# Kernel tuning notes

Measured on AMD Instinct MI355X. Metric: run time of the kernel, lower is better.

## Reference

```python
import jax, jax.numpy as jnp
import numpy as np

N, E = 50000, 800000
H, V, ED = 128, 32, 64
EH = 2 * H + 2 * V          # edge MLP hidden = 320
EO = 2 * H + 2 * V          # edge MLP out (H+H+V+V) = 320
NH = 2 * H + V              # node MLP hidden = 288
NO = H + V                  # node MLP out = 160


def _ln(x, g, b, eps=1e-5):
    m = x.mean(-1, keepdims=True)
    v = ((x - m) ** 2).mean(-1, keepdims=True)
    return (x - m) * jax.lax.rsqrt(v + eps) * g + b


def setup_inputs() -> dict:
    key = jax.random.key(0)
    ks = jax.random.split(key, 12)
    s = 0.05
    return {
        "scalar_state": jax.random.normal(ks[0], (N, H), jnp.float32),
        "vector_state": jax.random.normal(ks[1], (N, 3, V), jnp.float32),
        "edge_attr": jax.random.normal(ks[2], (E, ED), jnp.float32),
        "edge_vector": jax.random.normal(ks[3], (E, 3), jnp.float32),
        "sn_g": jnp.ones((H,), jnp.float32), "sn_b": jnp.zeros((H,), jnp.float32),
        "pn_g": jnp.ones((H,), jnp.float32), "pn_b": jnp.zeros((H,), jnp.float32),
        "e_w1": jax.random.normal(ks[4], (2 * H + ED, EH), jnp.float32) * s,
        "e_b1": jnp.zeros((EH,), jnp.float32),
        "e_w2": jax.random.normal(ks[5], (EH, EO), jnp.float32) * s,
        "e_b2": jnp.zeros((EO,), jnp.float32),
        "n_w1": jax.random.normal(ks[6], (H + V, NH), jnp.float32) * s,
        "n_b1": jnp.zeros((NH,), jnp.float32),
        "n_w2": jax.random.normal(ks[7], (NH, NO), jnp.float32) * s,
        "n_b2": jnp.zeros((NO,), jnp.float32),
        "edge_index": jax.random.randint(ks[8], (2, E), 0, N, jnp.int64),
    }


def reference(scalar_state, vector_state, edge_attr, edge_vector,
              sn_g, sn_b, pn_g, pn_b,
              e_w1, e_b1, e_w2, e_b2,
              n_w1, n_b1, n_w2, n_b2, edge_index):
    tgt = edge_index[0]
    src = edge_index[1]

    # LayerNorm is per-row, so normalize once then gather (same math as gather-then-norm)
    s_norm = _ln(scalar_state, sn_g, sn_b)
    edge_in = jnp.concatenate([s_norm[tgt], s_norm[src], edge_attr], axis=-1)  # [E, 2H+ED]
    h = jax.nn.silu(edge_in @ e_w1 + e_b1)
    upd = h @ e_w2 + e_b2                                                      # [E, 2H+2V]
    sm = upd[:, :H]
    sg = upd[:, H:2 * H]
    vg = upd[:, 2 * H:2 * H + V]
    ds = upd[:, 2 * H + V:]

    sm = sm * jax.nn.sigmoid(sg)                                               # scalar message [E,H]

    # F.normalize(edge_vector, dim=-1, eps=1e-8)
    ev_norm = jnp.sqrt((edge_vector ** 2).sum(-1, keepdims=True))
    unit = edge_vector / jnp.maximum(ev_norm, 1e-8)                            # [E,3]

    src_vec = vector_state[src] * jax.nn.sigmoid(vg)[:, None, :]               # [E,3,V]
    dir_vec = unit[:, :, None] * ds[:, None, :]                                # [E,3,V]
    vmsg = src_vec + dir_vec

    # mean aggregation (index_add / counts)
    counts = jax.ops.segment_sum(jnp.ones((E,), sm.dtype), tgt, num_segments=N)
    counts = jnp.maximum(counts, 1.0)
    s_upd = jax.ops.segment_sum(sm, tgt, num_segments=N) / counts[:, None]
    v_upd = jax.ops.segment_sum(vmsg.reshape(E, 3 * V), tgt, num_segments=N).reshape(N, 3, V) / counts[:, None, None]

    scalar_state = scalar_state + s_upd
    vector_state = vector_state + v_upd

    vnorm = jnp.sqrt(jnp.maximum((vector_state ** 2).sum(axis=1), 1e-8))       # [N,V]
    node_in = jnp.concatenate([_ln(scalar_state, pn_g, pn_b), vnorm], axis=-1)
    h2 = jax.nn.silu(node_in @ n_w1 + n_b1)
    nu = h2 @ n_w2 + n_b2                                                      # [N,H+V]
    scalar_delta = nu[:, :H]
    vector_scale = nu[:, H:]

    scalar_state = scalar_state + scalar_delta
    vector_state = vector_state * (1.0 + 0.1 * jnp.tanh(vector_scale))[:, None, :]
    return scalar_state, vector_state
```

## Files before the change

kernel.cpp:

```cpp
#include <hip/hip_runtime.h>

#define N_NODES 50000
#define N_EDGES 800000

typedef __attribute__((ext_vector_type(8))) short short8;
typedef __attribute__((ext_vector_type(4))) float floatx4;
typedef __attribute__((ext_vector_type(4))) unsigned int u32x4;
typedef unsigned short ushort_t;
typedef unsigned int uint_t;

__device__ __forceinline__ ushort_t f2bf(float f){
  unsigned u = __builtin_bit_cast(unsigned, f);
  u += 0x7fffu + ((u >> 16) & 1u);
  return (ushort_t)(u >> 16);
}
__device__ __forceinline__ float bf2f(ushort_t h){
  unsigned u = ((unsigned)h) << 16;
  return __builtin_bit_cast(float, u);
}
__device__ __forceinline__ uint_t pkbf(float lo, float hi){
#if __has_builtin(__builtin_amdgcn_cvt_pk_bf16_f32)
  typedef __attribute__((ext_vector_type(2))) __bf16 bf16x2;
  bf16x2 r = __builtin_amdgcn_cvt_pk_bf16_f32(lo, hi);
  return __builtin_bit_cast(uint_t, r);
#else
  return (uint_t)f2bf(lo) | ((uint_t)f2bf(hi) << 16);
#endif
}
__device__ __forceinline__ float sigm(float x){ return 1.f/(1.f+__expf(-x)); }
__device__ __forceinline__ float waveRed(float v){
  #pragma unroll
  for (int o=32;o>0;o>>=1) v += __shfl_xor(v,o);
  return v;
}
__device__ __forceinline__ int ldIdx(const int* __restrict__ idx, long long pos, int mode){
  return mode ? idx[pos*2] : idx[pos];
}
__device__ __forceinline__ short8 as_s8(u32x4 v){ return __builtin_bit_cast(short8, v); }

__device__ __forceinline__ void gl_lds16(const ushort_t* g, ushort_t* l){
  __builtin_amdgcn_global_load_lds(
    (const __attribute__((address_space(1))) unsigned int*)(unsigned long long)(uintptr_t)g,
    (__attribute__((address_space(3))) unsigned int*)(unsigned int)(uintptr_t)l,
    16, 0, 0);
}

__device__ __forceinline__ u32x4 bfadd8(u32x4 a, u32x4 b){
  u32x4 r;
  #pragma unroll
  for (int i=0;i<4;++i){
    float alo = __builtin_bit_cast(float, a[i]<<16);
    float ahi = __builtin_bit_cast(float, a[i]&0xffff0000u);
    float blo = __builtin_bit_cast(float, b[i]<<16);
    float bhi = __builtin_bit_cast(float, b[i]&0xffff0000u);
    r[i] = pkbf(alo+blo, ahi+bhi);
  }
  return r;
}
__device__ __forceinline__ short8 pack8(floatx4 x, floatx4 y){
  u32x4 u;
  u[0] = pkbf(x[0], x[1]); u[1] = pkbf(x[2], x[3]);
  u[2] = pkbf(y[0], y[1]); u[3] = pkbf(y[2], y[3]);
  return __builtin_bit_cast(short8, u);
}


__global__ void kDetect(const int* __restrict__ idx, int* __restrict__ flag){
  if (threadIdx.x==0 && blockIdx.x==0){
    int any = 0;
    for (int i=1;i<64;i+=2) any |= idx[i];
    *flag = (any==0) ? 1 : 0;
  }
}

__global__ void kLN(const float* __restrict__ s, const float* __restrict__ g,
                    const float* __restrict__ b, ushort_t* __restrict__ out, int N){
  int wid = threadIdx.x >> 6, lane = threadIdx.x & 63;
  int n = blockIdx.x*4 + wid;
  if (n >= N) return;
  float x0 = s[(size_t)n*128 + lane], x1 = s[(size_t)n*128 + 64 + lane];
  float sum = waveRed(x0 + x1);
  float sq  = waveRed(x0*x0 + x1*x1);
  float mean = sum * (1.f/128.f);
  float var  = sq * (1.f/128.f) - mean*mean;
  float rstd = rsqrtf(var + 1e-5f);
  out[(size_t)n*128 + lane]      = f2bf((x0-mean)*rstd*g[lane] + b[lane]);
  out[(size_t)n*128 + 64 + lane] = f2bf((x1-mean)*rstd*g[64+lane] + b[64+lane]);
}

__global__ void kReorder(const float* __restrict__ W, ushort_t* __restrict__ Wp,
                         int K, int OUT){
  int total = K*OUT;
  for (int o = blockIdx.x*blockDim.x + threadIdx.x; o < total; o += gridDim.x*blockDim.x){
    int j = o & 7; int rest = o >> 3;
    int nn = rest % OUT; int qk = rest / OUT;
    int q = qk & 3, kt = qk >> 2;
    int k = kt*32 + q*8 + j;
    Wp[o] = f2bf(W[(size_t)k*OUT + nn]);
  }
}

__global__ void kReorderAB(const float* __restrict__ W, ushort_t* __restrict__ Wp){
  int total = 128*640;
  for (int o = blockIdx.x*blockDim.x + threadIdx.x; o < total; o += gridDim.x*blockDim.x){
    int j = o & 7; int rest = o >> 3;
    int nn = rest % 640; int qk = rest / 640;
    int q = qk & 3, kt = qk >> 2;
    int k = kt*32 + q*8 + j;
    float v = (nn < 320) ? W[(size_t)k*320 + nn] : W[(size_t)(128+k)*320 + (nn-320)];
    Wp[o] = f2bf(v);
  }
}


__global__ void kHist(const int* __restrict__ idx, const int* __restrict__ flagp,
                      int* __restrict__ counts){
  int mode = *flagp;
  long long e = (long long)blockIdx.x*256 + threadIdx.x;
  if (e < N_EDGES) atomicAdd(&counts[ldIdx(idx, e, mode)], 1);
}

__global__ void kScanLocal(const int* __restrict__ counts, int* __restrict__ offsets,
                           int* __restrict__ bsum, int n){
  int tid = threadIdx.x, lane = tid & 63, wid = tid >> 6;
  int i = blockIdx.x*1024 + tid;
  int x = (i<n) ? counts[i] : 0;
  int v = x;
  #pragma unroll
  for (int o=1;o<64;o<<=1){ int t = __shfl_up(v,o); if (lane>=o) v += t; }
  __shared__ int ws[16];
  if (lane==63) ws[wid] = v;
  __syncthreads();
  if (wid==0){
    int s = (lane<16) ? ws[lane] : 0;
    #pragma unroll
    for (int o=1;o<16;o<<=1){ int t = __shfl_up(s,o); if (lane>=o) s += t; }
    if (lane<16) ws[lane] = s;
  }
  __syncthreads();
  int base = wid ? ws[wid-1] : 0;
  if (i<n) offsets[i] = base + v - x;
  if (tid==1023) bsum[blockIdx.x] = ws[15];
}
__global__ void kScanSums(const int* __restrict__ bsum, int* __restrict__ bbase, int nb){
  int lane = threadIdx.x;
  int x = (lane<nb) ? bsum[lane] : 0;
  int v = x;
  #pragma unroll
  for (int o=1;o<64;o<<=1){ int t = __shfl_up(v,o); if (lane>=o) v += t; }
  if (lane<nb) bbase[lane] = v - x;
}
__global__ void kScanAdd(int* __restrict__ offsets, int* __restrict__ cursor,
                         const int* __restrict__ bbase, int n){
  int i = blockIdx.x*1024 + threadIdx.x;
  if (i<n){ int v = offsets[i] + bbase[blockIdx.x]; offsets[i]=v; cursor[i]=v; }
}

__global__ void kScatter(const int* __restrict__ idx, const int* __restrict__ flagp,
                         int* __restrict__ cursor, const float* __restrict__ edge_vector,
                         int* __restrict__ sortedE, ushort_t* __restrict__ sortedT,
                         floatx4* __restrict__ aux){
  int mode = *flagp;
  long long e = (long long)blockIdx.x*256 + threadIdx.x;
  if (e < N_EDGES){
    int t = ldIdx(idx, e, mode);
    int s = ldIdx(idx, (long long)N_EDGES + e, mode);
    float ex = edge_vector[e*3], ey = edge_vector[e*3+1], ez = edge_vector[e*3+2];
    float inr = 1.f / fmaxf(sqrtf(ex*ex+ey*ey+ez*ez), 1e-8f);
    int pos = atomicAdd(&cursor[t], 1);
    sortedE[pos] = (int)e;
    sortedT[pos] = (ushort_t)t;
    floatx4 a; a[0] = __int_as_float(s); a[1] = ex*inr; a[2] = ey*inr; a[3] = ez*inr;
    aux[pos] = a;
  }
}

__global__ __launch_bounds__(256,2) void kNodeP(
  const ushort_t* __restrict__ s_norm, const ushort_t* __restrict__ Wabp,
  const float* __restrict__ b1, ushort_t* __restrict__ P)
{
  __shared__ u32x4 sA[1024];
  __shared__ u32x4 sB[2560];
  const int tid = threadIdx.x;
  const int lane = tid & 63, wid = tid >> 6;
  const int col = lane & 15, quad = lane >> 4;
  const int nb0 = blockIdx.x * 64;

  for (int i=0;i<4;++i){
    int d = i*256 + tid;
    int m=d&15, q=(d>>4)&3, mt=(d>>6)&3, kt=d>>8;
    int node = nb0 + mt*16 + m;
    u32x4 v = {0,0,0,0};
    if (node < N_NODES) v = *(const u32x4*)(s_norm + (size_t)node*128 + (kt*4+q)*8);
    sA[d] = v;
  }

  const floatx4 zz = {0.f,0.f,0.f,0.f};
  floatx4 acc[10][4];
  #pragma unroll
  for (int i=0;i<10;++i)
    #pragma unroll
    for (int j=0;j<4;++j) acc[i][j] = zz;

  for (int kt=0; kt<4; ++kt){
    for (int i=0;i<10;++i){
      int cb = i*256 + wid*64;
      gl_lds16(Wabp + ((size_t)kt*2560 + cb + lane)*8, (ushort_t*)&sB[cb]);
    }
    __syncthreads();
    short8 a[4];
    #pragma unroll
    for (int mt=0; mt<4; ++mt)
      a[mt] = as_s8(sA[((kt*4+mt)*4+quad)*16 + col]);
    #pragma unroll
    for (int nt=0; nt<10; ++nt){
      int n = wid*160 + nt*16 + col;
      short8 b = as_s8(sB[quad*640 + n]);
      #pragma unroll
      for (int mt=0; mt<4; ++mt)
        acc[nt][mt] = __builtin_amdgcn_mfma_f32_16x16x32_bf16(a[mt], b, acc[nt][mt], 0,0,0);
    }
    __syncthreads();
  }

  #pragma unroll
  for (int nt=0; nt<10; ++nt){
    int n = wid*160 + nt*16 + col;
    float bias = (n < 320) ? b1[n] : 0.f;
    #pragma unroll
    for (int mt=0; mt<4; ++mt)
      #pragma unroll
      for (int reg=0; reg<4; ++reg){
        int node = nb0 + mt*16 + quad*4 + reg;
        if (node < N_NODES)
          P[(size_t)node*640 + n] = f2bf(acc[nt][mt][reg] + bias);
      }
  }
}

__global__ __launch_bounds__(256,3) void kEdgeMLP(
    const ushort_t* __restrict__ P, const float* __restrict__ edge_attr,
    const ushort_t* __restrict__ W1cp, const ushort_t* __restrict__ W2p,
    const float* __restrict__ b2, const int* __restrict__ sortedE,
    const ushort_t* __restrict__ sortedT, const floatx4* __restrict__ aux,
    ushort_t* __restrict__ msg)
{
  __shared__ u32x4 sA[2560];
  __shared__ int sTgt[64], sSrc[64], sE[64];
  const int tid = threadIdx.x;
  const int lane = tid & 63, wid = tid >> 6;
  const int col = lane & 15, quad = lane >> 4;
  const long long p0 = (long long)blockIdx.x * 64;
  const int nb = wid * 80;

  if (tid < 64){
    sTgt[tid] = (int)sortedT[p0 + tid];
    sE[tid]   = sortedE[p0 + tid];
    sSrc[tid] = __float_as_int(aux[p0 + tid][0]);
  }
  __syncthreads();

  short8 aQ[2][4];
  #pragma unroll
  for (int kq=0; kq<2; ++kq)
    #pragma unroll
    for (int mt=0; mt<4; ++mt){
      const float* fp = edge_attr + (size_t)sE[mt*16+col]*64 + kq*32 + quad*8;
      aQ[kq][mt] = pack8(*(const floatx4*)fp, *(const floatx4*)(fp+4));
    }

  for (int i=0;i<10;++i){
    int d = i*256 + tid;
    int m=d&15, q=(d>>4)&3, mt=(d>>6)&3, kt=d>>8;
    int r = mt*16 + m;
    int n0 = kt*32 + q*8;
    u32x4 a = *(const u32x4*)(P + (size_t)sTgt[r]*640 + n0);
    u32x4 b = *(const u32x4*)(P + (size_t)sSrc[r]*640 + 320 + n0);
    sA[d] = bfadd8(a, b);
  }
  __syncthreads();

  const floatx4 zz = {0.f,0.f,0.f,0.f};
  floatx4 acc[5][4];
  #pragma unroll
  for (int i=0;i<5;++i)
    #pragma unroll
    for (int j=0;j<4;++j) acc[i][j] = zz;

  #pragma unroll
  for (int kq=0; kq<2; ++kq)
    #pragma unroll
    for (int nt=0; nt<5; ++nt){
      short8 b = as_s8(*(const u32x4*)(W1cp + ((size_t)(kq*4+quad)*320 + nb + nt*16 + col)*8));
      #pragma unroll
      for (int mt=0; mt<4; ++mt)
        acc[nt][mt] = __builtin_amdgcn_mfma_f32_16x16x32_bf16(aQ[kq][mt], b, acc[nt][mt], 0,0,0);
    }

  ushort_t* sH16 = (ushort_t*)sA;
  #pragma unroll
  for (int nt=0; nt<5; ++nt){
    int n = nb + nt*16 + col;
    int kt_h = n>>5, q_h = (n>>3)&3, j_h = n&7;
    #pragma unroll
    for (int mt=0; mt<4; ++mt)
      #pragma unroll
      for (int reg=0; reg<4; ++reg){
        int ml = quad*4 + reg;
        int a2 = (((kt_h*4 + mt)*4 + q_h)*16 + ml)*8 + j_h;
        float x = acc[nt][mt][reg] + bf2f(sH16[a2]);
        sH16[a2] = f2bf(x * sigm(x));
      }
  }
  #pragma unroll
  for (int i=0;i<5;++i)
    #pragma unroll
    for (int j=0;j<4;++j) acc[i][j] = zz;
  __syncthreads();

  const ushort_t* wb = W2p + ((size_t)quad*320 + nb + col)*8;
  for (int kt=0; kt<10; ++kt){
    short8 bfr[5];
    #pragma unroll
    for (int nt=0; nt<5; ++nt)
      bfr[nt] = as_s8(*(const u32x4*)(wb + (size_t)kt*10240 + nt*128));
    short8 a[4];
    #pragma unroll
    for (int mt=0; mt<4; ++mt)
      a[mt] = as_s8(sA[((kt*4+mt)*4+quad)*16 + col]);
    #pragma unroll
    for (int nt=0; nt<5; ++nt)
      #pragma unroll
      for (int mt=0; mt<4; ++mt)
        acc[nt][mt] = __builtin_amdgcn_mfma_f32_16x16x32_bf16(a[mt], bfr[nt], acc[nt][mt], 0,0,0);
  }
  __syncthreads();

  #pragma unroll
  for (int nt=0; nt<5; ++nt){
    int n = nb + nt*16 + col;
    float bias = b2[n];
    #pragma unroll
    for (int mt=0; mt<4; ++mt)
      #pragma unroll
      for (int reg=0; reg<4; ++reg){
        int mrow = mt*16 + quad*4 + reg;
        sH16[mrow*320 + n] = f2bf(acc[nt][mt][reg] + bias);
      }
  }
  __syncthreads();

  for (int pck = tid; pck < 6144; pck += 256){
    int r = pck / 96, u = pck % 96;
    float v0, v1;
    if (u < 64){
      int c0 = u*2;
      float a0 = bf2f(sH16[r*320 + c0]),   g0 = bf2f(sH16[r*320 + 128 + c0]);
      float a1 = bf2f(sH16[r*320 + c0+1]), g1 = bf2f(sH16[r*320 + 128 + c0+1]);
      v0 = a0 * sigm(g0); v1 = a1 * sigm(g1);
    } else if (u < 80){
      int vv = (u-64)*2;
      v0 = sigm(bf2f(sH16[r*320 + 256 + vv]));
      v1 = sigm(bf2f(sH16[r*320 + 256 + vv+1]));
    } else {
      int vv = (u-80)*2;
      v0 = bf2f(sH16[r*320 + 288 + vv]);
      v1 = bf2f(sH16[r*320 + 288 + vv+1]);
    }
    ((uint_t*)msg)[(size_t)(p0 + r)*96 + u] = pkbf(v0, v1);
  }
}

__global__ __launch_bounds__(128) void kAgg(
  const ushort_t* __restrict__ msg, const floatx4* __restrict__ aux,
  const int* __restrict__ counts, const int* __restrict__ offsets,
  const float* __restrict__ scalar_state, const float* __restrict__ vector_state,
  const float* __restrict__ pn_g, const float* __restrict__ pn_b,
  float* __restrict__ outS, float* __restrict__ outV, ushort_t* __restrict__ node_in)
{
  int n = blockIdx.x, t = threadIdx.x;
  int cnt = counts[n], start = offsets[n];
  int c = t >> 5, vv = t & 31;
  float accS = 0.f, accV = 0.f;
  for (int i=0; i<cnt; ++i){
    const ushort_t* row = msg + (size_t)(start+i)*192;
    accS += bf2f(row[t]);
    if (t < 96){
      floatx4 a = aux[start+i];
      int src = __float_as_int(a[0]);
      float sg  = bf2f(row[128+vv]);
      float dsv = bf2f(row[160+vv]);
      float sv = vector_state[(size_t)src*96 + t];
      float uc = (c==0) ? a[1] : (c==1) ? a[2] : a[3];
      accV += sv*sg + uc*dsv;
    }
  }
  float inv = 1.f / fmaxf((float)cnt, 1.f);
  __shared__ float lv[96];
  __shared__ float pS[2], pQ[2];
  float s1 = scalar_state[(size_t)n*128 + t] + accS*inv;
  outS[(size_t)n*128 + t] = s1;
  if (t < 96){
    float v1 = vector_state[(size_t)n*96 + t] + accV*inv;
    outV[(size_t)n*96 + t] = v1;
    lv[t] = v1;
  }
  float wsum = waveRed(s1), wsq = waveRed(s1*s1);
  if ((t&63)==0){ pS[t>>6]=wsum; pQ[t>>6]=wsq; }
  __syncthreads();
  float mean = (pS[0]+pS[1]) * (1.f/128.f);
  float var  = (pQ[0]+pQ[1]) * (1.f/128.f) - mean*mean;
  float rstd = rsqrtf(var + 1e-5f);
  node_in[(size_t)n*160 + t] = f2bf((s1-mean)*rstd*pn_g[t] + pn_b[t]);
  if (t < 32){
    float a = lv[t], b = lv[32+t], d = lv[64+t];
    float vn = sqrtf(fmaxf(a*a+b*b+d*d, 1e-8f));
    node_in[(size_t)n*160 + 128 + t] = f2bf(vn);
  }
}

__global__ __launch_bounds__(256,2) void kNodeMLP(
  const ushort_t* __restrict__ node_in, const ushort_t* __restrict__ W1np,
  const ushort_t* __restrict__ W2np, const float* __restrict__ b1,
  const float* __restrict__ b2, float* __restrict__ outS, float* __restrict__ outV)
{
  __shared__ u32x4 sA[640];
  __shared__ u32x4 sH[1152];
  const int tid = threadIdx.x;
  const int lane = tid & 63, wid = tid >> 6;
  const int col = lane & 15, quad = lane >> 4;
  const int wm = wid & 1, wn = wid >> 1;
  const int rbase = blockIdx.x * 32;

  for (int d = tid; d < 640; d += 256){
    int m = d & 15, q = (d>>4)&3, mtile = (d>>6)&1, kt = d>>7;
    int r = rbase + mtile*16 + m, cc = kt*4 + q;
    u32x4 v = {0,0,0,0};
    if (r < N_NODES) v = *(const u32x4*)(node_in + (size_t)r*160 + cc*8);
    sA[d] = v;
  }
  __syncthreads();

  const floatx4 zz = {0.f,0.f,0.f,0.f};
  floatx4 acc[9];
  #pragma unroll
  for (int i=0;i<9;++i) acc[i] = zz;

  for (int kt=0; kt<5; ++kt){
    short8 a = as_s8(sA[((kt*2+wm)*4+quad)*16 + col]);
    #pragma unroll
    for (int jt=0; jt<9; ++jt){
      int n = wn*144 + jt*16 + col;
      short8 b = as_s8(*(const u32x4*)(W1np + (size_t)kt*9216 + ((size_t)quad*288 + n)*8));
      acc[jt] = __builtin_amdgcn_mfma_f32_16x16x32_bf16(a, b, acc[jt], 0,0,0);
    }
  }
  ushort_t* sH16 = (ushort_t*)sH;
  #pragma unroll
  for (int jt=0; jt<9; ++jt){
    int n = wn*144 + jt*16 + col;
    float bias = b1[n];
    int kt_h = n>>5, q_h = (n>>3)&3, j_h = n&7;
    #pragma unroll
    for (int reg=0; reg<4; ++reg){
      int ml = quad*4 + reg;
      float x = acc[jt][reg] + bias;
      float s = x * sigm(x);
      int chunk = ((kt_h*2 + wm)*4 + q_h)*16 + ml;
      sH16[chunk*8 + j_h] = f2bf(s);
    }
  }
  __syncthreads();

  floatx4 acc2[5];
  #pragma unroll
  for (int i=0;i<5;++i) acc2[i] = zz;

  for (int kt=0; kt<9; ++kt){
    short8 a = as_s8(sH[((kt*2+wm)*4+quad)*16 + col]);
    #pragma unroll
    for (int jt=0; jt<5; ++jt){
      int n = wn*80 + jt*16 + col;
      short8 b = as_s8(*(const u32x4*)(W2np + (size_t)kt*5120 + ((size_t)quad*160 + n)*8));
      acc2[jt] = __builtin_amdgcn_mfma_f32_16x16x32_bf16(a, b, acc2[jt], 0,0,0);
    }
  }

  #pragma unroll
  for (int jt=0; jt<5; ++jt){
    int n = wn*80 + jt*16 + col;
    float bias = b2[n];
    #pragma unroll
    for (int reg=0; reg<4; ++reg){
      int ml = quad*4 + reg;
      int r = rbase + wm*16 + ml;
      if (r < N_NODES){
        float val = acc2[jt][reg] + bias;
        if (n < 128){
          float* o = outS + (size_t)r*128 + n;
          *o = *o + val;
        } else {
          int vv = n - 128;
          float f = 1.f + 0.1f * tanhf(val);
          float* o = outV + (size_t)r*96 + vv;
          o[0] *= f; o[32] *= f; o[64] *= f;
        }
      }
    }
  }
}


extern "C" void kernel_launch(void* const* d_in, const int* in_sizes, int n_in,
                              void* d_out, int out_size, void* d_ws, size_t ws_size,
                              hipStream_t stream)
{
  const float* scalar_state = (const float*)d_in[0];
  const float* vector_state = (const float*)d_in[1];
  const float* edge_attr    = (const float*)d_in[2];
  const float* edge_vector  = (const float*)d_in[3];
  const float* sn_g = (const float*)d_in[4];
  const float* sn_b = (const float*)d_in[5];
  const float* pn_g = (const float*)d_in[6];
  const float* pn_b = (const float*)d_in[7];
  const float* e_w1 = (const float*)d_in[8];
  const float* e_b1 = (const float*)d_in[9];
  const float* e_w2 = (const float*)d_in[10];
  const float* e_b2 = (const float*)d_in[11];
  const float* n_w1 = (const float*)d_in[12];
  const float* n_b1 = (const float*)d_in[13];
  const float* n_w2 = (const float*)d_in[14];
  const float* n_b2 = (const float*)d_in[15];
  const int*   eidx = (const int*)d_in[16];

  char* p = (char*)d_ws;
  auto take = [&](size_t bytes)->char*{
    char* r = p; p += (bytes + 255) & ~(size_t)255; return r;
  };
  int*      flag    = (int*)take(4);
  ushort_t* s_norm  = (ushort_t*)take((size_t)N_NODES*128*2);
  ushort_t* Wabp    = (ushort_t*)take((size_t)128*640*2);
  ushort_t* W1cp    = (ushort_t*)take((size_t)64*320*2);
  ushort_t* W2p     = (ushort_t*)take((size_t)320*320*2);
  ushort_t* W1np    = (ushort_t*)take((size_t)160*288*2);
  ushort_t* W2np    = (ushort_t*)take((size_t)288*160*2);
  int*      counts  = (int*)take((size_t)N_NODES*4);
  int*      offsets = (int*)take((size_t)N_NODES*4);
  int*      cursor  = (int*)take((size_t)N_NODES*4);
  int*      bsum    = (int*)take(64*4);
  int*      bbase   = (int*)take(64*4);
  int*      sortedE = (int*)take((size_t)N_EDGES*4);
  ushort_t* sortedT = (ushort_t*)take((size_t)N_EDGES*2);
  floatx4*  aux     = (floatx4*)take((size_t)N_EDGES*16);
  ushort_t* Pbuf    = (ushort_t*)take((size_t)N_NODES*640*2);
  ushort_t* msg     = (ushort_t*)take((size_t)N_EDGES*192*2);
  ushort_t* node_in = Pbuf;
  (void)ws_size; (void)in_sizes; (void)n_in; (void)out_size;

  float* outS = (float*)d_out;
  float* outV = outS + (size_t)N_NODES*128;

  kDetect<<<1, 64, 0, stream>>>(eidx, flag);
  kLN<<<(N_NODES+3)/4, 256, 0, stream>>>(scalar_state, sn_g, sn_b, s_norm, N_NODES);
  kReorderAB<<<160, 256, 0, stream>>>(e_w1, Wabp);
  kReorder<<<160, 256, 0, stream>>>(e_w1 + (size_t)256*320, W1cp, 64, 320);
  kReorder<<<160, 256, 0, stream>>>(e_w2, W2p, 320, 320);
  kReorder<<<160, 256, 0, stream>>>(n_w1, W1np, 160, 288);
  kReorder<<<160, 256, 0, stream>>>(n_w2, W2np, 288, 160);
  hipMemsetAsync(counts, 0, (size_t)N_NODES*4, stream);
  kHist<<<N_EDGES/256, 256, 0, stream>>>(eidx, flag, counts);
  int nsb = (N_NODES + 1023)/1024;
  kScanLocal<<<nsb, 1024, 0, stream>>>(counts, offsets, bsum, N_NODES);
  kScanSums<<<1, 64, 0, stream>>>(bsum, bbase, nsb);
  kScanAdd<<<nsb, 1024, 0, stream>>>(offsets, cursor, bbase, N_NODES);
  kScatter<<<N_EDGES/256, 256, 0, stream>>>(eidx, flag, cursor, edge_vector,
                                            sortedE, sortedT, aux);
  kNodeP<<<(N_NODES+63)/64, 256, 0, stream>>>(s_norm, Wabp, e_b1, Pbuf);
  kEdgeMLP<<<N_EDGES/64, 256, 0, stream>>>(Pbuf, edge_attr, W1cp, W2p,
                                           e_b2, sortedE, sortedT, aux, msg);
  kAgg<<<N_NODES, 128, 0, stream>>>(msg, aux, counts, offsets,
                                    scalar_state, vector_state,
                                    pn_g, pn_b, outS, outV, node_in);
  kNodeMLP<<<(N_NODES+31)/32, 256, 0, stream>>>(node_in, W1np, W2np, n_b1, n_b2, outS, outV);
}
```

Before: 1.237 ms.

## Remap edge MLP output columns so gating epilogue runs in registers

The edge MLP now gives each wave output columns so that the message column and its gate column (n and n+128) sit in the same lane's accumulators. The sigmoid gating and the bf16 message store can then be done straight from registers. This removes the LDS staging of the full 64x320 output, two block barriers and the repacking loop. It also loads edge indices straight into registers instead of through shared memory, and swaps in hardware rcp based sigmoid/tanh and native bf16 conversions. The trade-offs are narrow scattered 2-byte global stores of msg and slightly lower accuracy in the fast reciprocal and tanh.

```diff
diff --git a/kernel.cpp b/kernel.cpp
--- a/kernel.cpp
+++ b/kernel.cpp
@@ -6,28 +6,29 @@
 typedef __attribute__((ext_vector_type(8))) short short8;
 typedef __attribute__((ext_vector_type(4))) float floatx4;
 typedef __attribute__((ext_vector_type(4))) unsigned int u32x4;
+typedef __attribute__((ext_vector_type(2))) __bf16 bf16x2;
 typedef unsigned short ushort_t;
 typedef unsigned int uint_t;
 
+__device__ __forceinline__ uint_t pkbf(float lo, float hi){
+  bf16x2 v = { (__bf16)lo, (__bf16)hi };
+  return __builtin_bit_cast(uint_t, v);
+}
 __device__ __forceinline__ ushort_t f2bf(float f){
-  unsigned u = __builtin_bit_cast(unsigned, f);
-  u += 0x7fffu + ((u >> 16) & 1u);
-  return (ushort_t)(u >> 16);
+  return __builtin_bit_cast(ushort_t, (__bf16)f);
 }
 __device__ __forceinline__ float bf2f(ushort_t h){
   unsigned u = ((unsigned)h) << 16;
   return __builtin_bit_cast(float, u);
 }
-__device__ __forceinline__ uint_t pkbf(float lo, float hi){
-#if __has_builtin(__builtin_amdgcn_cvt_pk_bf16_f32)
-  typedef __attribute__((ext_vector_type(2))) __bf16 bf16x2;
-  bf16x2 r = __builtin_amdgcn_cvt_pk_bf16_f32(lo, hi);
-  return __builtin_bit_cast(uint_t, r);
-#else
-  return (uint_t)f2bf(lo) | ((uint_t)f2bf(hi) << 16);
-#endif
-}
-__device__ __forceinline__ float sigm(float x){ return 1.f/(1.f+__expf(-x)); }
+__device__ __forceinline__ float sigm(float x){
+  return __builtin_amdgcn_rcpf(1.f + __expf(-x));
+}
+__device__ __forceinline__ float tanh_f(float x){
+  float ax = fabsf(x);
+  float t = 1.f - 2.f*__builtin_amdgcn_rcpf(__expf(2.f*ax) + 1.f);
+  return copysignf(t, x);
+}
 __device__ __forceinline__ float waveRed(float v){
   #pragma unroll
   for (int o=32;o>0;o>>=1) v += __shfl_xor(v,o);
@@ -246,37 +247,40 @@
     ushort_t* __restrict__ msg)
 {
   __shared__ u32x4 sA[2560];
-  __shared__ int sTgt[64], sSrc[64], sE[64];
   const int tid = threadIdx.x;
   const int lane = tid & 63, wid = tid >> 6;
   const int col = lane & 15, quad = lane >> 4;
   const long long p0 = (long long)blockIdx.x * 64;
-  const int nb = wid * 80;
-
-  if (tid < 64){
-    sTgt[tid] = (int)sortedT[p0 + tid];
-    sE[tid]   = sortedE[p0 + tid];
-    sSrc[tid] = __float_as_int(aux[p0 + tid][0]);
-  }
-  __syncthreads();
+
+  int ncol[5];
+  ncol[0] = wid*32 + col;
+  ncol[1] = ncol[0] + 16;
+  ncol[2] = ncol[0] + 128;
+  ncol[3] = ncol[0] + 144;
+  ncol[4] = 256 + wid*16 + col;
+
+  int eId[4];
+  #pragma unroll
+  for (int mt=0;mt<4;++mt) eId[mt] = sortedE[p0 + mt*16 + col];
 
   short8 aQ[2][4];
   #pragma unroll
   for (int kq=0; kq<2; ++kq)
     #pragma unroll
     for (int mt=0; mt<4; ++mt){
-      const float* fp = edge_attr + (size_t)sE[mt*16+col]*64 + kq*32 + quad*8;
+      const float* fp = edge_attr + (size_t)eId[mt]*64 + kq*32 + quad*8;
       aQ[kq][mt] = pack8(*(const floatx4*)fp, *(const floatx4*)(fp+4));
     }
 
-  for (int i=0;i<10;++i){
-    int d = i*256 + tid;
-    int m=d&15, q=(d>>4)&3, mt=(d>>6)&3, kt=d>>8;
-    int r = mt*16 + m;
-    int n0 = kt*32 + q*8;
-    u32x4 a = *(const u32x4*)(P + (size_t)sTgt[r]*640 + n0);
-    u32x4 b = *(const u32x4*)(P + (size_t)sSrc[r]*640 + 320 + n0);
-    sA[d] = bfadd8(a, b);
+  {
+    const int r = wid*16 + col;
+    int tgt = (int)sortedT[p0 + r];
+    int src = __float_as_int(((const float*)aux)[(size_t)(p0 + r)*4]);
+    const u32x4* pT = (const u32x4*)(P + (size_t)tgt*640) + quad;
+    const u32x4* pS = (const u32x4*)(P + (size_t)src*640 + 320) + quad;
+    #pragma unroll
+    for (int i=0;i<10;++i)
+      sA[i*256 + tid] = bfadd8(pT[i*4], pS[i*4]);
   }
   __syncthreads();
 
@@ -291,7 +295,7 @@
   for (int kq=0; kq<2; ++kq)
     #pragma unroll
     for (int nt=0; nt<5; ++nt){
-      short8 b = as_s8(*(const u32x4*)(W1cp + ((size_t)(kq*4+quad)*320 + nb + nt*16 + col)*8));
+      short8 b = as_s8(*(const u32x4*)(W1cp + ((size_t)(kq*4+quad)*320 + ncol[nt])*8));
       #pragma unroll
       for (int mt=0; mt<4; ++mt)
         acc[nt][mt] = __builtin_amdgcn_mfma_f32_16x16x32_bf16(aQ[kq][mt], b, acc[nt][mt], 0,0,0);
@@ -300,16 +304,15 @@
   ushort_t* sH16 = (ushort_t*)sA;
   #pragma unroll
   for (int nt=0; nt<5; ++nt){
-    int n = nb + nt*16 + col;
-    int kt_h = n>>5, q_h = (n>>3)&3, j_h = n&7;
+    int n = ncol[nt];
+    ushort_t* hp = sH16 + (((n>>5)*256 + ((n>>3)&3)*16 + quad*4)*8 + (n&7));
     #pragma unroll
     for (int mt=0; mt<4; ++mt)
       #pragma unroll
       for (int reg=0; reg<4; ++reg){
-        int ml = quad*4 + reg;
-        int a2 = (((kt_h*4 + mt)*4 + q_h)*16 + ml)*8 + j_h;
-        float x = acc[nt][mt][reg] + bf2f(sH16[a2]);
-        sH16[a2] = f2bf(x * sigm(x));
+        int a2 = mt*512 + reg*8;
+        float x = acc[nt][mt][reg] + bf2f(hp[a2]);
+        hp[a2] = f2bf(x * sigm(x));
       }
   }
   #pragma unroll
@@ -318,12 +321,16 @@
     for (int j=0;j<4;++j) acc[i][j] = zz;
   __syncthreads();
 
-  const ushort_t* wb = W2p + ((size_t)quad*320 + nb + col)*8;
+  float b2c[5];
+  #pragma unroll
+  for (int nt=0;nt<5;++nt) b2c[nt] = b2[ncol[nt]];
+
+  const ushort_t* w2q = W2p + (size_t)quad*320*8;
   for (int kt=0; kt<10; ++kt){
     short8 bfr[5];
     #pragma unroll
     for (int nt=0; nt<5; ++nt)
-      bfr[nt] = as_s8(*(const u32x4*)(wb + (size_t)kt*10240 + nt*128));
+      bfr[nt] = as_s8(*(const u32x4*)(w2q + (size_t)kt*10240 + (size_t)ncol[nt]*8));
     short8 a[4];
     #pragma unroll
     for (int mt=0; mt<4; ++mt)
@@ -334,41 +341,23 @@
       for (int mt=0; mt<4; ++mt)
         acc[nt][mt] = __builtin_amdgcn_mfma_f32_16x16x32_bf16(a[mt], bfr[nt], acc[nt][mt], 0,0,0);
   }
-  __syncthreads();
-
-  #pragma unroll
-  for (int nt=0; nt<5; ++nt){
-    int n = nb + nt*16 + col;
-    float bias = b2[n];
-    #pragma unroll
-    for (int mt=0; mt<4; ++mt)
-      #pragma unroll
-      for (int reg=0; reg<4; ++reg){
-        int mrow = mt*16 + quad*4 + reg;
-        sH16[mrow*320 + n] = f2bf(acc[nt][mt][reg] + bias);
-      }
-  }
-  __syncthreads();
-
-  for (int pck = tid; pck < 6144; pck += 256){
-    int r = pck / 96, u = pck % 96;
-    float v0, v1;
-    if (u < 64){
-      int c0 = u*2;
-      float a0 = bf2f(sH16[r*320 + c0]),   g0 = bf2f(sH16[r*320 + 128 + c0]);
-      float a1 = bf2f(sH16[r*320 + c0+1]), g1 = bf2f(sH16[r*320 + 128 + c0+1]);
-      v0 = a0 * sigm(g0); v1 = a1 * sigm(g1);
-    } else if (u < 80){
-      int vv = (u-64)*2;
-      v0 = sigm(bf2f(sH16[r*320 + 256 + vv]));
-      v1 = sigm(bf2f(sH16[r*320 + 256 + vv+1]));
-    } else {
-      int vv = (u-80)*2;
-      v0 = bf2f(sH16[r*320 + 288 + vv]);
-      v1 = bf2f(sH16[r*320 + 288 + vv+1]);
-    }
-    ((uint_t*)msg)[(size_t)(p0 + r)*96 + u] = pkbf(v0, v1);
-  }
+
+  #pragma unroll
+  for (int mt=0; mt<4; ++mt)
+    #pragma unroll
+    for (int reg=0; reg<4; ++reg){
+      int row = mt*16 + quad*4 + reg;
+      ushort_t* mrow = msg + (size_t)(p0 + row)*192;
+      float a0 = acc[0][mt][reg] + b2c[0];
+      float g0 = acc[2][mt][reg] + b2c[2];
+      mrow[ncol[0]] = f2bf(a0 * sigm(g0));
+      float a1 = acc[1][mt][reg] + b2c[1];
+      float g1 = acc[3][mt][reg] + b2c[3];
+      mrow[ncol[1]] = f2bf(a1 * sigm(g1));
+      float v4 = acc[4][mt][reg] + b2c[4];
+      float ov = (wid < 2) ? sigm(v4) : v4;
+      mrow[ncol[4] - 128] = f2bf(ov);
+    }
 }
 
 __global__ __launch_bounds__(128) void kAgg(
@@ -501,7 +490,7 @@
           *o = *o + val;
         } else {
           int vv = n - 128;
-          float f = 1.f + 0.1f * tanhf(val);
+          float f = 1.f + 0.1f * tanh_f(val);
           float* o = outV + (size_t)r*96 + vv;
           o[0] *= f; o[32] *= f; o[64] *= f;
         }
```

Result: faster. 1.079 ms (-12.8%).
